# Optimization experiments

Hardware: AMD Instinct MI355X
Metric: run time of the kernel (lower is better)

The kernel has to match this reference:

```python
import jax, jax.numpy as jnp
import numpy as np

N_NODES = 100000
N_EDGES = 1600000
D_IN = 256
D_OUT = 64
BN_EPS = 1e-5


def setup_inputs() -> dict:
    key = jax.random.key(0)
    ks = jax.random.split(key, 8)
    x = jax.random.normal(ks[0], (N_NODES, D_IN), dtype=jnp.float32)
    edge_index = jax.random.randint(ks[1], (2, N_EDGES), 0, N_NODES, dtype=jnp.int32)
    W = jax.random.normal(ks[2], (D_OUT, D_IN), dtype=jnp.float32) / np.sqrt(D_IN).astype(np.float32)
    bias = 0.01 * jax.random.normal(ks[3], (D_OUT,), dtype=jnp.float32)
    gamma = 1.0 + 0.1 * jax.random.normal(ks[4], (D_OUT,), dtype=jnp.float32)
    beta = 0.1 * jax.random.normal(ks[5], (D_OUT,), dtype=jnp.float32)
    running_mean = 0.1 * jax.random.normal(ks[6], (D_OUT,), dtype=jnp.float32)
    running_var = jax.random.uniform(ks[7], (D_OUT,), dtype=jnp.float32, minval=0.5, maxval=1.5)
    return {"x": x, "edge_index": edge_index, "W": W, "bias": bias,
            "gamma": gamma, "beta": beta,
            "running_mean": running_mean, "running_var": running_var}


def reference(x, edge_index, W, bias, gamma, beta, running_mean, running_var):
    # GCNConv (PyG semantics): transform -> symmetric-normalized scatter-add with
    # self-loops (edge_weight = ones, self-loop weight = 1), then +bias.
    n = x.shape[0]
    loop = jnp.arange(n, dtype=edge_index.dtype)
    row = jnp.concatenate([edge_index[0], loop])  # source nodes
    col = jnp.concatenate([edge_index[1], loop])  # target nodes
    w = jnp.ones(row.shape[0], dtype=x.dtype)
    deg = jax.ops.segment_sum(w, col, num_segments=n)          # [N]
    dinv = jnp.where(deg > 0, jax.lax.rsqrt(deg), 0.0)          # D^{-1/2}
    norm = dinv[row] * w * dinv[col]                            # [E+N]
    xw = x @ W.T                                                # [N, D_OUT]
    agg = jax.ops.segment_sum(norm[:, None] * xw[row], col, num_segments=n)
    out = agg + bias
    # BatchNorm1d in eval mode (running stats); dropout inactive in eval.
    out = (out - running_mean) * jax.lax.rsqrt(running_var + BN_EPS) * gamma + beta
    return jax.nn.relu(out)
```

## Files before the change

kernel.cpp:

```cpp
#include <hip/hip_runtime.h>
#include <hip/hip_bf16.h>

#define D_IN 256
#define D_OUT 64
#define BN_EPS 1e-5f

#define BINSHIFT 8
#define BINCAP 4608
#define PCHUNK 8192

typedef __attribute__((ext_vector_type(4))) float floatx4;
typedef __attribute__((ext_vector_type(8))) __bf16 bf16x8;
typedef __attribute__((ext_vector_type(4))) unsigned uintx4;

__global__ __launch_bounds__(256) void k_prep(
        const float* __restrict__ W, __bf16* __restrict__ whi, __bf16* __restrict__ wlo,
        const float* __restrict__ bias, const float* __restrict__ gamma,
        const float* __restrict__ beta, const float* __restrict__ rmean,
        const float* __restrict__ rvar,
        float* __restrict__ bnsc, float* __restrict__ bnsh,
        int* __restrict__ bincur, int nbins) {
    int b = blockIdx.x, t = threadIdx.x;
    if (b < 2) {
        int i = b * 256 + t;
        if (i < nbins) bincur[i] = 0;
        if (b == 1 && t < D_OUT) {
            float sc = rsqrtf(rvar[t] + BN_EPS) * gamma[t];
            bnsc[t] = sc;
            bnsh[t] = (bias[t] - rmean[t]) * sc + beta[t];
        }
        return;
    }
    int tid = (b - 2) * 256 + t;
    int lane = tid & 63, c = (tid >> 6) & 7, tt = tid >> 9;
    int row = tt * 16 + (lane & 15);
    int k0 = c * 32 + (lane >> 4) * 8;
    size_t dst = (size_t)tid * 8;
    #pragma unroll
    for (int j = 0; j < 8; ++j) {
        float w = W[(size_t)row * D_IN + k0 + j];
        __bf16 h = (__bf16)w;
        whi[dst + j] = h;
        wlo[dst + j] = (__bf16)(w - (float)h);
    }
}

__global__ __launch_bounds__(256) void k_part(
        const int* __restrict__ ei, int* __restrict__ bincur,
        unsigned* __restrict__ pairs, int E, int nbins) {
    __shared__ int hist[512];
    __shared__ int base[512];
    int t = threadIdx.x;
    int e0 = blockIdx.x * PCHUNK;

    for (int j = t; j < nbins; j += 256) hist[j] = 0;
    __syncthreads();

    int cols[PCHUNK / 256];
    int ranks[PCHUNK / 256];
    #pragma unroll
    for (int i = 0; i < PCHUNK / 256; ++i) {
        int e = e0 + i * 256 + t;
        if (e < E) {
            int c = ei[E + e];
            cols[i] = c;
            ranks[i] = atomicAdd(&hist[c >> BINSHIFT], 1);
        }
    }
    __syncthreads();
    for (int j = t; j < nbins; j += 256)
        base[j] = atomicAdd(&bincur[j], hist[j]);
    __syncthreads();
    #pragma unroll
    for (int i = 0; i < PCHUNK / 256; ++i) {
        int e = e0 + i * 256 + t;
        if (e < E) {
            int c = cols[i];
            int bin = c >> BINSHIFT;
            int pos = base[bin] + ranks[i];
            if (pos >= BINCAP) pos = BINCAP - 1;
            pairs[(size_t)bin * BINCAP + pos] =
                ((unsigned)ei[e] << 8) | (unsigned)(c & 255);
        }
    }
}

__global__ __launch_bounds__(256) void k_fill3(
        const unsigned* __restrict__ pairs, const int* __restrict__ bincur,
        int* __restrict__ off, float* __restrict__ dinv,
        int* __restrict__ srcs, int n, int nbins) {
    __shared__ int hist[256];
    __shared__ int sc[256];
    __shared__ int curs[256];
    __shared__ int sbase;
    int bin = blockIdx.x, t = threadIdx.x;

    int i0 = 2 * t, i1 = 2 * t + 1;
    int v0 = (i0 < nbins) ? bincur[i0] : 0;
    int v1 = (i1 < nbins) ? bincur[i1] : 0;
    int s = v0 + v1;
    sc[t] = s;
    hist[t] = 0;
    __syncthreads();
    for (int o = 1; o < 256; o <<= 1) {
        int v = (t >= o) ? sc[t - o] : 0;
        __syncthreads();
        sc[t] += v;
        __syncthreads();
    }
    int excl = sc[t] - s;
    if (t == (bin >> 1)) sbase = (bin & 1) ? (excl + v0) : excl;
    if (bin == 0 && t == 255) off[n] = sc[255];
    __syncthreads();
    int binoff_b = sbase;

    int cnt = bincur[bin];
    const unsigned* bp = pairs + (size_t)bin * BINCAP;
    for (int p = t; p < cnt; p += 256)
        atomicAdd(&hist[bp[p] & 255u], 1);
    __syncthreads();
    int own = hist[t];
    sc[t] = own;
    __syncthreads();
    for (int o = 1; o < 256; o <<= 1) {
        int v = (t >= o) ? sc[t - o] : 0;
        __syncthreads();
        sc[t] += v;
        __syncthreads();
    }
    int base = binoff_b + sc[t] - own;
    int node = (bin << BINSHIFT) + t;
    curs[t] = base;
    if (node < n) {
        off[node] = base;
        dinv[node] = rsqrtf((float)(own + 1));
    }
    __syncthreads();
    for (int p = t; p < cnt; p += 256) {
        unsigned v = bp[p];
        int pos = atomicAdd(&curs[v & 255u], 1);
        srcs[pos] = (int)(v >> 8);
    }
}

__global__ __launch_bounds__(256) void k_gemm(
        const float* __restrict__ x, const __bf16* __restrict__ whi,
        const __bf16* __restrict__ wlo, const float* __restrict__ dinv,
        __bf16* __restrict__ yb, int n) {
    int wave = threadIdx.x >> 6;
    int lane = threadIdx.x & 63;
    int m0 = blockIdx.x * 64 + wave * 16;
    if (m0 >= n) return;
    int q = lane >> 4, cl = lane & 15;
    int arow = m0 + cl; if (arow >= n) arow = n - 1;
    const float* ap = x + (size_t)arow * D_IN + q * 8;

    floatx4 acc[4] = {{0.f,0.f,0.f,0.f},{0.f,0.f,0.f,0.f},
                      {0.f,0.f,0.f,0.f},{0.f,0.f,0.f,0.f}};

    #pragma unroll
    for (int c = 0; c < 8; ++c) {
        floatx4 a0 = *(const floatx4*)(ap + c * 32);
        floatx4 a1 = *(const floatx4*)(ap + c * 32 + 4);
        bf16x8 ahi, alo;
        #pragma unroll
        for (int j = 0; j < 4; ++j) {
            __bf16 h0 = (__bf16)a0[j];
            __bf16 h1 = (__bf16)a1[j];
            ahi[j] = h0;     alo[j] = (__bf16)(a0[j] - (float)h0);
            ahi[4 + j] = h1; alo[4 + j] = (__bf16)(a1[j] - (float)h1);
        }
        #pragma unroll
        for (int t = 0; t < 4; ++t) {
            size_t fo = ((size_t)(t * 8 + c) * 64 + lane) * 8;
            bf16x8 bh = *(const bf16x8*)(whi + fo);
            bf16x8 bl = *(const bf16x8*)(wlo + fo);
            acc[t] = __builtin_amdgcn_mfma_f32_16x16x32_bf16(ahi, bh, acc[t], 0, 0, 0);
            acc[t] = __builtin_amdgcn_mfma_f32_16x16x32_bf16(alo, bh, acc[t], 0, 0, 0);
            acc[t] = __builtin_amdgcn_mfma_f32_16x16x32_bf16(ahi, bl, acc[t], 0, 0, 0);
        }
    }

    int nb = m0 + q * 4;
    float dv[4];
    #pragma unroll
    for (int r = 0; r < 4; ++r) dv[r] = (nb + r < n) ? dinv[nb + r] : 0.f;
    #pragma unroll
    for (int t = 0; t < 4; ++t) {
        #pragma unroll
        for (int r = 0; r < 4; ++r) {
            int node = nb + r;
            if (node < n)
                yb[(size_t)node * D_OUT + t * 16 + cl] = (__bf16)(dv[r] * acc[t][r]);
        }
    }
}

__device__ __forceinline__ void acc_row4(uintx4 v, float (&a)[8]) {
    #pragma unroll
    for (int k = 0; k < 4; ++k) {
        a[2 * k]     += __uint_as_float(v[k] << 16);
        a[2 * k + 1] += __uint_as_float(v[k] & 0xffff0000u);
    }
}

__global__ __launch_bounds__(256) void k_aggregate(
        const int* __restrict__ off, const int* __restrict__ srcs,
        const unsigned* __restrict__ ybf, const float* __restrict__ dinv,
        const float* __restrict__ bnsc, const float* __restrict__ bnsh,
        float* __restrict__ out, int n) {
    int node = blockIdx.x * 4 + (threadIdx.x >> 6);
    if (node >= n) return;
    int lane = threadIdx.x & 63;
    int g = lane >> 3, sl = lane & 7;
    int s = off[node], e2 = off[node + 1];

    float a[8] = {0.f, 0.f, 0.f, 0.f, 0.f, 0.f, 0.f, 0.f};
    float dv = 0.f;
    floatx4 bs0, bs1, bh0, bh1;
    if (g == 0) {
        dv = dinv[node];
        bs0 = *(const floatx4*)(bnsc + sl * 8);
        bs1 = *(const floatx4*)(bnsc + sl * 8 + 4);
        bh0 = *(const floatx4*)(bnsh + sl * 8);
        bh1 = *(const floatx4*)(bnsh + sl * 8 + 4);
        uintx4 v = *(const uintx4*)(ybf + (size_t)node * 32 + sl * 4);
        acc_row4(v, a);
    }

    int e = s + g;
    for (; e + 24 < e2; e += 32) {
        int r0 = srcs[e], r1 = srcs[e + 8], r2 = srcs[e + 16], r3 = srcs[e + 24];
        uintx4 v0 = *(const uintx4*)(ybf + (size_t)r0 * 32 + sl * 4);
        uintx4 v1 = *(const uintx4*)(ybf + (size_t)r1 * 32 + sl * 4);
        uintx4 v2 = *(const uintx4*)(ybf + (size_t)r2 * 32 + sl * 4);
        uintx4 v3 = *(const uintx4*)(ybf + (size_t)r3 * 32 + sl * 4);
        acc_row4(v0, a);
        acc_row4(v1, a);
        acc_row4(v2, a);
        acc_row4(v3, a);
    }
    for (; e + 8 < e2; e += 16) {
        int r0 = srcs[e], r1 = srcs[e + 8];
        uintx4 v0 = *(const uintx4*)(ybf + (size_t)r0 * 32 + sl * 4);
        uintx4 v1 = *(const uintx4*)(ybf + (size_t)r1 * 32 + sl * 4);
        acc_row4(v0, a);
        acc_row4(v1, a);
    }
    for (; e < e2; e += 8) {
        uintx4 v = *(const uintx4*)(ybf + (size_t)srcs[e] * 32 + sl * 4);
        acc_row4(v, a);
    }

    #pragma unroll
    for (int k = 0; k < 8; ++k) {
        a[k] += __shfl_xor(a[k], 8);
        a[k] += __shfl_xor(a[k], 16);
        a[k] += __shfl_xor(a[k], 32);
    }

    if (g == 0) {
        float o[8];
        #pragma unroll
        for (int k = 0; k < 4; ++k) {
            o[k]     = fmaf(dv * a[k],     bs0[k], bh0[k]);
            o[4 + k] = fmaf(dv * a[4 + k], bs1[k], bh1[k]);
        }
        floatx4 w0 = { fmaxf(o[0], 0.f), fmaxf(o[1], 0.f),
                       fmaxf(o[2], 0.f), fmaxf(o[3], 0.f) };
        floatx4 w1 = { fmaxf(o[4], 0.f), fmaxf(o[5], 0.f),
                       fmaxf(o[6], 0.f), fmaxf(o[7], 0.f) };
        *(floatx4*)(out + (size_t)node * D_OUT + sl * 8) = w0;
        *(floatx4*)(out + (size_t)node * D_OUT + sl * 8 + 4) = w1;
    }
}

static inline char* align_up(char* p, size_t a) {
    return (char*)(((uintptr_t)p + a - 1) & ~(uintptr_t)(a - 1));
}

extern "C" void kernel_launch(void* const* d_in, const int* in_sizes, int n_in,
                              void* d_out, int out_size, void* d_ws, size_t ws_size,
                              hipStream_t stream) {
    const float* x     = (const float*)d_in[0];
    const int*   ei    = (const int*)d_in[1];
    const float* W     = (const float*)d_in[2];
    const float* bias  = (const float*)d_in[3];
    const float* gamma = (const float*)d_in[4];
    const float* beta  = (const float*)d_in[5];
    const float* rmean = (const float*)d_in[6];
    const float* rvar  = (const float*)d_in[7];
    float* out = (float*)d_out;

    int N = in_sizes[0] / D_IN;
    int E = in_sizes[1] / 2;
    int nbins = (N + (1 << BINSHIFT) - 1) >> BINSHIFT;

    char* p = (char*)d_ws;
    int*      bincur = (int*)p;         p += 512 * 4;
    int*      off    = (int*)p;         p += (size_t)(N + 1) * 4; p = align_up(p, 256);
    float*    dinv   = (float*)p;       p += (size_t)N * 4;       p = align_up(p, 256);
    float*    bnsc   = (float*)p;       p += D_OUT * 4;
    float*    bnsh   = (float*)p;       p += D_OUT * 4;           p = align_up(p, 256);
    __bf16*   whi    = (__bf16*)p;      p += (size_t)D_OUT * D_IN * 2; p = align_up(p, 256);
    __bf16*   wlo    = (__bf16*)p;      p += (size_t)D_OUT * D_IN * 2; p = align_up(p, 256);
    __bf16*   yb     = (__bf16*)p;      p += (size_t)N * D_OUT * 2;    p = align_up(p, 256);
    int*      srcs   = (int*)p;         p += (size_t)E * 4;       p = align_up(p, 256);
    unsigned* pairs  = (unsigned*)p;

    k_prep<<<10, 256, 0, stream>>>(W, whi, wlo, bias, gamma, beta, rmean, rvar,
                                   bnsc, bnsh, bincur, nbins);
    k_part<<<(E + PCHUNK - 1) / PCHUNK, 256, 0, stream>>>(ei, bincur, pairs, E, nbins);
    k_fill3<<<nbins, 256, 0, stream>>>(pairs, bincur, off, dinv, srcs, N, nbins);
    k_gemm<<<(N + 63) / 64, 256, 0, stream>>>(x, whi, wlo, dinv, yb, N);
    k_aggregate<<<(N + 3) / 4, 256, 0, stream>>>(off, srcs, (const unsigned*)yb,
                                                 dinv, bnsc, bnsh, out, N);
}
```

Before: 287.0 us.

## Drop CSR build; aggregate directly from 64-node bins with LDS atomics

```diff
diff --git a/kernel.cpp b/kernel.cpp
--- a/kernel.cpp
+++ b/kernel.cpp
@@ -5,8 +5,8 @@
 #define D_OUT 64
 #define BN_EPS 1e-5f
 
-#define BINSHIFT 8
-#define BINCAP 4608
+#define BINSHIFT 6
+#define BINCAP 1536
 #define PCHUNK 8192
 
 typedef __attribute__((ext_vector_type(4))) float floatx4;
@@ -19,37 +19,45 @@
         const float* __restrict__ beta, const float* __restrict__ rmean,
         const float* __restrict__ rvar,
         float* __restrict__ bnsc, float* __restrict__ bnsh,
-        int* __restrict__ bincur, int nbins) {
+        int* __restrict__ bincur, int* __restrict__ deg, int nbins, int N) {
     int b = blockIdx.x, t = threadIdx.x;
-    if (b < 2) {
+    if (b < 8) {
         int i = b * 256 + t;
         if (i < nbins) bincur[i] = 0;
-        if (b == 1 && t < D_OUT) {
+        return;
+    }
+    if (b == 8) {
+        if (t < D_OUT) {
             float sc = rsqrtf(rvar[t] + BN_EPS) * gamma[t];
             bnsc[t] = sc;
             bnsh[t] = (bias[t] - rmean[t]) * sc + beta[t];
         }
         return;
     }
-    int tid = (b - 2) * 256 + t;
-    int lane = tid & 63, c = (tid >> 6) & 7, tt = tid >> 9;
-    int row = tt * 16 + (lane & 15);
-    int k0 = c * 32 + (lane >> 4) * 8;
-    size_t dst = (size_t)tid * 8;
-    #pragma unroll
-    for (int j = 0; j < 8; ++j) {
-        float w = W[(size_t)row * D_IN + k0 + j];
-        __bf16 h = (__bf16)w;
-        whi[dst + j] = h;
-        wlo[dst + j] = (__bf16)(w - (float)h);
-    }
+    if (b < 17) {
+        int tid = (b - 9) * 256 + t;
+        int lane = tid & 63, c = (tid >> 6) & 7, tt = tid >> 9;
+        int row = tt * 16 + (lane & 15);
+        int k0 = c * 32 + (lane >> 4) * 8;
+        size_t dst = (size_t)tid * 8;
+        #pragma unroll
+        for (int j = 0; j < 8; ++j) {
+            float w = W[(size_t)row * D_IN + k0 + j];
+            __bf16 h = (__bf16)w;
+            whi[dst + j] = h;
+            wlo[dst + j] = (__bf16)(w - (float)h);
+        }
+        return;
+    }
+    int stride = (gridDim.x - 17) * 256;
+    for (int i = (b - 17) * 256 + t; i < N; i += stride) deg[i] = 0;
 }
 
 __global__ __launch_bounds__(256) void k_part(
-        const int* __restrict__ ei, int* __restrict__ bincur,
+        const int* __restrict__ ei, int* __restrict__ bincur, int* __restrict__ deg,
         unsigned* __restrict__ pairs, int E, int nbins) {
-    __shared__ int hist[512];
-    __shared__ int base[512];
+    __shared__ int hist[2048];
+    __shared__ int base[2048];
     int t = threadIdx.x;
     int e0 = blockIdx.x * PCHUNK;
 
@@ -65,11 +73,14 @@
             int c = ei[E + e];
             cols[i] = c;
             ranks[i] = atomicAdd(&hist[c >> BINSHIFT], 1);
-        }
-    }
-    __syncthreads();
-    for (int j = t; j < nbins; j += 256)
-        base[j] = atomicAdd(&bincur[j], hist[j]);
+            atomicAdd(&deg[c], 1);
+        }
+    }
+    __syncthreads();
+    for (int j = t; j < nbins; j += 256) {
+        int h = hist[j];
+        base[j] = h ? atomicAdd(&bincur[j], h) : 0;
+    }
     __syncthreads();
     #pragma unroll
     for (int i = 0; i < PCHUNK / 256; ++i) {
@@ -80,72 +91,14 @@
             int pos = base[bin] + ranks[i];
             if (pos >= BINCAP) pos = BINCAP - 1;
             pairs[(size_t)bin * BINCAP + pos] =
-                ((unsigned)ei[e] << 8) | (unsigned)(c & 255);
-        }
-    }
-}
-
-__global__ __launch_bounds__(256) void k_fill3(
-        const unsigned* __restrict__ pairs, const int* __restrict__ bincur,
-        int* __restrict__ off, float* __restrict__ dinv,
-        int* __restrict__ srcs, int n, int nbins) {
-    __shared__ int hist[256];
-    __shared__ int sc[256];
-    __shared__ int curs[256];
-    __shared__ int sbase;
-    int bin = blockIdx.x, t = threadIdx.x;
-
-    int i0 = 2 * t, i1 = 2 * t + 1;
-    int v0 = (i0 < nbins) ? bincur[i0] : 0;
-    int v1 = (i1 < nbins) ? bincur[i1] : 0;
-    int s = v0 + v1;
-    sc[t] = s;
-    hist[t] = 0;
-    __syncthreads();
-    for (int o = 1; o < 256; o <<= 1) {
-        int v = (t >= o) ? sc[t - o] : 0;
-        __syncthreads();
-        sc[t] += v;
-        __syncthreads();
-    }
-    int excl = sc[t] - s;
-    if (t == (bin >> 1)) sbase = (bin & 1) ? (excl + v0) : excl;
-    if (bin == 0 && t == 255) off[n] = sc[255];
-    __syncthreads();
-    int binoff_b = sbase;
-
-    int cnt = bincur[bin];
-    const unsigned* bp = pairs + (size_t)bin * BINCAP;
-    for (int p = t; p < cnt; p += 256)
-        atomicAdd(&hist[bp[p] & 255u], 1);
-    __syncthreads();
-    int own = hist[t];
-    sc[t] = own;
-    __syncthreads();
-    for (int o = 1; o < 256; o <<= 1) {
-        int v = (t >= o) ? sc[t - o] : 0;
-        __syncthreads();
-        sc[t] += v;
-        __syncthreads();
-    }
-    int base = binoff_b + sc[t] - own;
-    int node = (bin << BINSHIFT) + t;
-    curs[t] = base;
-    if (node < n) {
-        off[node] = base;
-        dinv[node] = rsqrtf((float)(own + 1));
-    }
-    __syncthreads();
-    for (int p = t; p < cnt; p += 256) {
-        unsigned v = bp[p];
-        int pos = atomicAdd(&curs[v & 255u], 1);
-        srcs[pos] = (int)(v >> 8);
+                ((unsigned)ei[e] << BINSHIFT) | (unsigned)(c & 63);
+        }
     }
 }
 
 __global__ __launch_bounds__(256) void k_gemm(
         const float* __restrict__ x, const __bf16* __restrict__ whi,
-        const __bf16* __restrict__ wlo, const float* __restrict__ dinv,
+        const __bf16* __restrict__ wlo, const int* __restrict__ deg,
         __bf16* __restrict__ yb, int n) {
     int wave = threadIdx.x >> 6;
     int lane = threadIdx.x & 63;
@@ -184,7 +137,8 @@
     int nb = m0 + q * 4;
     float dv[4];
     #pragma unroll
-    for (int r = 0; r < 4; ++r) dv[r] = (nb + r < n) ? dinv[nb + r] : 0.f;
+    for (int r = 0; r < 4; ++r)
+        dv[r] = (nb + r < n) ? rsqrtf((float)(deg[nb + r] + 1)) : 0.f;
     #pragma unroll
     for (int t = 0; t < 4; ++t) {
         #pragma unroll
@@ -196,82 +150,74 @@
     }
 }
 
-__device__ __forceinline__ void acc_row4(uintx4 v, float (&a)[8]) {
-    #pragma unroll
-    for (int k = 0; k < 4; ++k) {
-        a[2 * k]     += __uint_as_float(v[k] << 16);
-        a[2 * k + 1] += __uint_as_float(v[k] & 0xffff0000u);
-    }
-}
-
 __global__ __launch_bounds__(256) void k_aggregate(
-        const int* __restrict__ off, const int* __restrict__ srcs,
-        const unsigned* __restrict__ ybf, const float* __restrict__ dinv,
+        const unsigned* __restrict__ pairs, const int* __restrict__ bincur,
+        const int* __restrict__ deg, const unsigned* __restrict__ ybf,
         const float* __restrict__ bnsc, const float* __restrict__ bnsh,
         float* __restrict__ out, int n) {
-    int node = blockIdx.x * 4 + (threadIdx.x >> 6);
-    if (node >= n) return;
-    int lane = threadIdx.x & 63;
-    int g = lane >> 3, sl = lane & 7;
-    int s = off[node], e2 = off[node + 1];
-
-    float a[8] = {0.f, 0.f, 0.f, 0.f, 0.f, 0.f, 0.f, 0.f};
-    float dv = 0.f;
-    floatx4 bs0, bs1, bh0, bh1;
-    if (g == 0) {
-        dv = dinv[node];
-        bs0 = *(const floatx4*)(bnsc + sl * 8);
-        bs1 = *(const floatx4*)(bnsc + sl * 8 + 4);
-        bh0 = *(const floatx4*)(bnsh + sl * 8);
-        bh1 = *(const floatx4*)(bnsh + sl * 8 + 4);
-        uintx4 v = *(const uintx4*)(ybf + (size_t)node * 32 + sl * 4);
-        acc_row4(v, a);
-    }
-
-    int e = s + g;
-    for (; e + 24 < e2; e += 32) {
-        int r0 = srcs[e], r1 = srcs[e + 8], r2 = srcs[e + 16], r3 = srcs[e + 24];
-        uintx4 v0 = *(const uintx4*)(ybf + (size_t)r0 * 32 + sl * 4);
-        uintx4 v1 = *(const uintx4*)(ybf + (size_t)r1 * 32 + sl * 4);
-        uintx4 v2 = *(const uintx4*)(ybf + (size_t)r2 * 32 + sl * 4);
-        uintx4 v3 = *(const uintx4*)(ybf + (size_t)r3 * 32 + sl * 4);
-        acc_row4(v0, a);
-        acc_row4(v1, a);
-        acc_row4(v2, a);
-        acc_row4(v3, a);
-    }
-    for (; e + 8 < e2; e += 16) {
-        int r0 = srcs[e], r1 = srcs[e + 8];
-        uintx4 v0 = *(const uintx4*)(ybf + (size_t)r0 * 32 + sl * 4);
-        uintx4 v1 = *(const uintx4*)(ybf + (size_t)r1 * 32 + sl * 4);
-        acc_row4(v0, a);
-        acc_row4(v1, a);
-    }
-    for (; e < e2; e += 8) {
-        uintx4 v = *(const uintx4*)(ybf + (size_t)srcs[e] * 32 + sl * 4);
-        acc_row4(v, a);
-    }
-
-    #pragma unroll
-    for (int k = 0; k < 8; ++k) {
-        a[k] += __shfl_xor(a[k], 8);
-        a[k] += __shfl_xor(a[k], 16);
-        a[k] += __shfl_xor(a[k], 32);
-    }
-
-    if (g == 0) {
-        float o[8];
+    __shared__ float acc[64][64];
+    int bin = blockIdx.x, t = threadIdx.x;
+
+    float* fa = (float*)acc;
+    #pragma unroll
+    for (int i = 0; i < 16; ++i) fa[t + i * 256] = 0.f;
+    __syncthreads();
+
+    int cnt = bincur[bin]; if (cnt > BINCAP) cnt = BINCAP;
+    const unsigned* bp = pairs + (size_t)bin * BINCAP;
+    int g = t >> 3, sl = t & 7;
+
+    int p = g;
+    for (; p + 32 < cnt; p += 64) {
+        unsigned pr0 = bp[p], pr1 = bp[p + 32];
+        uintx4 v0 = *(const uintx4*)(ybf + (size_t)(pr0 >> BINSHIFT) * 32 + sl * 4);
+        uintx4 v1 = *(const uintx4*)(ybf + (size_t)(pr1 >> BINSHIFT) * 32 + sl * 4);
+        int t0 = pr0 & 63, t1 = pr1 & 63;
         #pragma unroll
         for (int k = 0; k < 4; ++k) {
-            o[k]     = fmaf(dv * a[k],     bs0[k], bh0[k]);
-            o[4 + k] = fmaf(dv * a[4 + k], bs1[k], bh1[k]);
-        }
-        floatx4 w0 = { fmaxf(o[0], 0.f), fmaxf(o[1], 0.f),
-                       fmaxf(o[2], 0.f), fmaxf(o[3], 0.f) };
-        floatx4 w1 = { fmaxf(o[4], 0.f), fmaxf(o[5], 0.f),
-                       fmaxf(o[6], 0.f), fmaxf(o[7], 0.f) };
-        *(floatx4*)(out + (size_t)node * D_OUT + sl * 8) = w0;
-        *(floatx4*)(out + (size_t)node * D_OUT + sl * 8 + 4) = w1;
+            atomicAdd(&acc[t0][sl * 8 + 2 * k],     __uint_as_float(v0[k] << 16));
+            atomicAdd(&acc[t0][sl * 8 + 2 * k + 1], __uint_as_float(v0[k] & 0xffff0000u));
+        }
+        #pragma unroll
+        for (int k = 0; k < 4; ++k) {
+            atomicAdd(&acc[t1][sl * 8 + 2 * k],     __uint_as_float(v1[k] << 16));
+            atomicAdd(&acc[t1][sl * 8 + 2 * k + 1], __uint_as_float(v1[k] & 0xffff0000u));
+        }
+    }
+    for (; p < cnt; p += 32) {
+        unsigned pr = bp[p];
+        uintx4 v = *(const uintx4*)(ybf + (size_t)(pr >> BINSHIFT) * 32 + sl * 4);
+        int tl = pr & 63;
+        #pragma unroll
+        for (int k = 0; k < 4; ++k) {
+            atomicAdd(&acc[tl][sl * 8 + 2 * k],     __uint_as_float(v[k] << 16));
+            atomicAdd(&acc[tl][sl * 8 + 2 * k + 1], __uint_as_float(v[k] & 0xffff0000u));
+        }
+    }
+    __syncthreads();
+
+    int nl = t >> 2, ch0 = (t & 3) * 16;
+    int node = (bin << BINSHIFT) + nl;
+    if (node < n) {
+        float dv = rsqrtf((float)(deg[node] + 1));
+        const unsigned* yr = ybf + (size_t)node * 32 + (t & 3) * 8;
+        #pragma unroll
+        for (int j = 0; j < 4; ++j) {
+            unsigned u0 = yr[2 * j], u1 = yr[2 * j + 1];
+            float s0 = acc[nl][ch0 + 4 * j + 0] + __uint_as_float(u0 << 16);
+            float s1 = acc[nl][ch0 + 4 * j + 1] + __uint_as_float(u0 & 0xffff0000u);
+            float s2 = acc[nl][ch0 + 4 * j + 2] + __uint_as_float(u1 << 16);
+            float s3 = acc[nl][ch0 + 4 * j + 3] + __uint_as_float(u1 & 0xffff0000u);
+            floatx4 bs = *(const floatx4*)(bnsc + ch0 + 4 * j);
+            floatx4 bh = *(const floatx4*)(bnsh + ch0 + 4 * j);
+            float o0 = fmaf(dv * s0, bs[0], bh[0]);
+            float o1 = fmaf(dv * s1, bs[1], bh[1]);
+            float o2 = fmaf(dv * s2, bs[2], bh[2]);
+            float o3 = fmaf(dv * s3, bs[3], bh[3]);
+            floatx4 w = { fmaxf(o0, 0.f), fmaxf(o1, 0.f),
+                          fmaxf(o2, 0.f), fmaxf(o3, 0.f) };
+            *(floatx4*)(out + (size_t)node * D_OUT + ch0 + 4 * j) = w;
+        }
     }
 }
 
@@ -297,22 +243,19 @@
     int nbins = (N + (1 << BINSHIFT) - 1) >> BINSHIFT;
 
     char* p = (char*)d_ws;
-    int*      bincur = (int*)p;         p += 512 * 4;
-    int*      off    = (int*)p;         p += (size_t)(N + 1) * 4; p = align_up(p, 256);
-    float*    dinv   = (float*)p;       p += (size_t)N * 4;       p = align_up(p, 256);
+    int*      bincur = (int*)p;         p += 2048 * 4;
+    int*      deg    = (int*)p;         p += (size_t)N * 4;       p = align_up(p, 256);
     float*    bnsc   = (float*)p;       p += D_OUT * 4;
     float*    bnsh   = (float*)p;       p += D_OUT * 4;           p = align_up(p, 256);
     __bf16*   whi    = (__bf16*)p;      p += (size_t)D_OUT * D_IN * 2; p = align_up(p, 256);
     __bf16*   wlo    = (__bf16*)p;      p += (size_t)D_OUT * D_IN * 2; p = align_up(p, 256);
     __bf16*   yb     = (__bf16*)p;      p += (size_t)N * D_OUT * 2;    p = align_up(p, 256);
-    int*      srcs   = (int*)p;         p += (size_t)E * 4;       p = align_up(p, 256);
     unsigned* pairs  = (unsigned*)p;
 
-    k_prep<<<10, 256, 0, stream>>>(W, whi, wlo, bias, gamma, beta, rmean, rvar,
-                                   bnsc, bnsh, bincur, nbins);
-    k_part<<<(E + PCHUNK - 1) / PCHUNK, 256, 0, stream>>>(ei, bincur, pairs, E, nbins);
-    k_fill3<<<nbins, 256, 0, stream>>>(pairs, bincur, off, dinv, srcs, N, nbins);
-    k_gemm<<<(N + 63) / 64, 256, 0, stream>>>(x, whi, wlo, dinv, yb, N);
-    k_aggregate<<<(N + 3) / 4, 256, 0, stream>>>(off, srcs, (const unsigned*)yb,
-                                                 dinv, bnsc, bnsh, out, N);
-}
+    k_prep<<<115, 256, 0, stream>>>(W, whi, wlo, bias, gamma, beta, rmean, rvar,
+                                    bnsc, bnsh, bincur, deg, nbins, N);
+    k_part<<<(E + PCHUNK - 1) / PCHUNK, 256, 0, stream>>>(ei, bincur, deg, pairs, E, nbins);
+    k_gemm<<<(N + 63) / 64, 256, 0, stream>>>(x, whi, wlo, deg, yb, N);
+    k_aggregate<<<nbins, 256, 0, stream>>>(pairs, bincur, deg, (const unsigned*)yb,
+                                           bnsc, bnsh, out, N);
+}
```

After: 877.0 us. 206% more time.

## Split transformed features into four column slabs and aggregate each in separate passes

Applied to the files above, without the earlier changes.

```diff
diff --git a/kernel.cpp b/kernel.cpp
--- a/kernel.cpp
+++ b/kernel.cpp
@@ -11,7 +11,6 @@
 
 typedef __attribute__((ext_vector_type(4))) float floatx4;
 typedef __attribute__((ext_vector_type(8))) __bf16 bf16x8;
-typedef __attribute__((ext_vector_type(4))) unsigned uintx4;
 
 __global__ __launch_bounds__(256) void k_prep(
         const float* __restrict__ W, __bf16* __restrict__ whi, __bf16* __restrict__ wlo,
@@ -146,7 +145,7 @@
 __global__ __launch_bounds__(256) void k_gemm(
         const float* __restrict__ x, const __bf16* __restrict__ whi,
         const __bf16* __restrict__ wlo, const float* __restrict__ dinv,
-        __bf16* __restrict__ yb, int n) {
+        __bf16* __restrict__ ys, int n) {
     int wave = threadIdx.x >> 6;
     int lane = threadIdx.x & 63;
     int m0 = blockIdx.x * 64 + wave * 16;
@@ -191,87 +190,82 @@
         for (int r = 0; r < 4; ++r) {
             int node = nb + r;
             if (node < n)
-                yb[(size_t)node * D_OUT + t * 16 + cl] = (__bf16)(dv[r] * acc[t][r]);
-        }
-    }
-}
-
-__device__ __forceinline__ void acc_row4(uintx4 v, float (&a)[8]) {
-    #pragma unroll
-    for (int k = 0; k < 4; ++k) {
-        a[2 * k]     += __uint_as_float(v[k] << 16);
-        a[2 * k + 1] += __uint_as_float(v[k] & 0xffff0000u);
-    }
-}
-
-__global__ __launch_bounds__(256) void k_aggregate(
+                ys[((size_t)t * n + node) * 16 + cl] = (__bf16)(dv[r] * acc[t][r]);
+        }
+    }
+}
+
+__device__ __forceinline__ void acc_row(uint2 v, float& a0, float& a1,
+                                        float& a2, float& a3) {
+    a0 += __uint_as_float(v.x << 16);
+    a1 += __uint_as_float(v.x & 0xffff0000u);
+    a2 += __uint_as_float(v.y << 16);
+    a3 += __uint_as_float(v.y & 0xffff0000u);
+}
+
+__global__ __launch_bounds__(256) void k_agg(
         const int* __restrict__ off, const int* __restrict__ srcs,
-        const unsigned* __restrict__ ybf, const float* __restrict__ dinv,
+        const unsigned* __restrict__ yq, const float* __restrict__ dinv,
         const float* __restrict__ bnsc, const float* __restrict__ bnsh,
-        float* __restrict__ out, int n) {
+        float* __restrict__ out, int n, int q) {
     int node = blockIdx.x * 4 + (threadIdx.x >> 6);
     if (node >= n) return;
     int lane = threadIdx.x & 63;
-    int g = lane >> 3, sl = lane & 7;
+    int g = lane >> 2, sl = lane & 3;
     int s = off[node], e2 = off[node + 1];
 
-    float a[8] = {0.f, 0.f, 0.f, 0.f, 0.f, 0.f, 0.f, 0.f};
+    float a0 = 0.f, a1 = 0.f, a2 = 0.f, a3 = 0.f;
     float dv = 0.f;
-    floatx4 bs0, bs1, bh0, bh1;
+    floatx4 bs, bh;
     if (g == 0) {
         dv = dinv[node];
-        bs0 = *(const floatx4*)(bnsc + sl * 8);
-        bs1 = *(const floatx4*)(bnsc + sl * 8 + 4);
-        bh0 = *(const floatx4*)(bnsh + sl * 8);
-        bh1 = *(const floatx4*)(bnsh + sl * 8 + 4);
-        uintx4 v = *(const uintx4*)(ybf + (size_t)node * 32 + sl * 4);
-        acc_row4(v, a);
+        bs = *(const floatx4*)(bnsc + q * 16 + sl * 4);
+        bh = *(const floatx4*)(bnsh + q * 16 + sl * 4);
+        uint2 v = *(const uint2*)(yq + (size_t)node * 8 + sl * 2);
+        acc_row(v, a0, a1, a2, a3);
     }
 
     int e = s + g;
-    for (; e + 24 < e2; e += 32) {
-        int r0 = srcs[e], r1 = srcs[e + 8], r2 = srcs[e + 16], r3 = srcs[e + 24];
-        uintx4 v0 = *(const uintx4*)(ybf + (size_t)r0 * 32 + sl * 4);
-        uintx4 v1 = *(const uintx4*)(ybf + (size_t)r1 * 32 + sl * 4);
-        uintx4 v2 = *(const uintx4*)(ybf + (size_t)r2 * 32 + sl * 4);
-        uintx4 v3 = *(const uintx4*)(ybf + (size_t)r3 * 32 + sl * 4);
-        acc_row4(v0, a);
-        acc_row4(v1, a);
-        acc_row4(v2, a);
-        acc_row4(v3, a);
-    }
-    for (; e + 8 < e2; e += 16) {
-        int r0 = srcs[e], r1 = srcs[e + 8];
-        uintx4 v0 = *(const uintx4*)(ybf + (size_t)r0 * 32 + sl * 4);
-        uintx4 v1 = *(const uintx4*)(ybf + (size_t)r1 * 32 + sl * 4);
-        acc_row4(v0, a);
-        acc_row4(v1, a);
-    }
-    for (; e < e2; e += 8) {
-        uintx4 v = *(const uintx4*)(ybf + (size_t)srcs[e] * 32 + sl * 4);
-        acc_row4(v, a);
-    }
-
-    #pragma unroll
-    for (int k = 0; k < 8; ++k) {
-        a[k] += __shfl_xor(a[k], 8);
-        a[k] += __shfl_xor(a[k], 16);
-        a[k] += __shfl_xor(a[k], 32);
-    }
+    for (; e + 48 < e2; e += 64) {
+        int r0 = srcs[e], r1 = srcs[e + 16], r2 = srcs[e + 32], r3 = srcs[e + 48];
+        uint2 v0 = *(const uint2*)(yq + (size_t)r0 * 8 + sl * 2);
+        uint2 v1 = *(const uint2*)(yq + (size_t)r1 * 8 + sl * 2);
+        uint2 v2 = *(const uint2*)(yq + (size_t)r2 * 8 + sl * 2);
+        uint2 v3 = *(const uint2*)(yq + (size_t)r3 * 8 + sl * 2);
+        acc_row(v0, a0, a1, a2, a3);
+        acc_row(v1, a0, a1, a2, a3);
+        acc_row(v2, a0, a1, a2, a3);
+        acc_row(v3, a0, a1, a2, a3);
+    }
+    for (; e + 16 < e2; e += 32) {
+        int r0 = srcs[e], r1 = srcs[e + 16];
+        uint2 v0 = *(const uint2*)(yq + (size_t)r0 * 8 + sl * 2);
+        uint2 v1 = *(const uint2*)(yq + (size_t)r1 * 8 + sl * 2);
+        acc_row(v0, a0, a1, a2, a3);
+        acc_row(v1, a0, a1, a2, a3);
+    }
+    for (; e < e2; e += 16) {
+        uint2 v = *(const uint2*)(yq + (size_t)srcs[e] * 8 + sl * 2);
+        acc_row(v, a0, a1, a2, a3);
+    }
+
+    a0 += __shfl_xor(a0, 4);  a1 += __shfl_xor(a1, 4);
+    a2 += __shfl_xor(a2, 4);  a3 += __shfl_xor(a3, 4);
+    a0 += __shfl_xor(a0, 8);  a1 += __shfl_xor(a1, 8);
+    a2 += __shfl_xor(a2, 8);  a3 += __shfl_xor(a3, 8);
+    a0 += __shfl_xor(a0, 16); a1 += __shfl_xor(a1, 16);
+    a2 += __shfl_xor(a2, 16); a3 += __shfl_xor(a3, 16);
+    a0 += __shfl_xor(a0, 32); a1 += __shfl_xor(a1, 32);
+    a2 += __shfl_xor(a2, 32); a3 += __shfl_xor(a3, 32);
 
     if (g == 0) {
-        float o[8];
-        #pragma unroll
-        for (int k = 0; k < 4; ++k) {
-            o[k]     = fmaf(dv * a[k],     bs0[k], bh0[k]);
-            o[4 + k] = fmaf(dv * a[4 + k], bs1[k], bh1[k]);
-        }
-        floatx4 w0 = { fmaxf(o[0], 0.f), fmaxf(o[1], 0.f),
-                       fmaxf(o[2], 0.f), fmaxf(o[3], 0.f) };
-        floatx4 w1 = { fmaxf(o[4], 0.f), fmaxf(o[5], 0.f),
-                       fmaxf(o[6], 0.f), fmaxf(o[7], 0.f) };
-        *(floatx4*)(out + (size_t)node * D_OUT + sl * 8) = w0;
-        *(floatx4*)(out + (size_t)node * D_OUT + sl * 8 + 4) = w1;
+        float o0 = fmaf(dv * a0, bs[0], bh[0]);
+        float o1 = fmaf(dv * a1, bs[1], bh[1]);
+        float o2 = fmaf(dv * a2, bs[2], bh[2]);
+        float o3 = fmaf(dv * a3, bs[3], bh[3]);
+        floatx4 o = { o0 > 0.f ? o0 : 0.f, o1 > 0.f ? o1 : 0.f,
+                      o2 > 0.f ? o2 : 0.f, o3 > 0.f ? o3 : 0.f };
+        *(floatx4*)(out + (size_t)node * D_OUT + q * 16 + sl * 4) = o;
     }
 }
 
@@ -304,7 +298,7 @@
     float*    bnsh   = (float*)p;       p += D_OUT * 4;           p = align_up(p, 256);
     __bf16*   whi    = (__bf16*)p;      p += (size_t)D_OUT * D_IN * 2; p = align_up(p, 256);
     __bf16*   wlo    = (__bf16*)p;      p += (size_t)D_OUT * D_IN * 2; p = align_up(p, 256);
-    __bf16*   yb     = (__bf16*)p;      p += (size_t)N * D_OUT * 2;    p = align_up(p, 256);
+    __bf16*   ys     = (__bf16*)p;      p += (size_t)N * D_OUT * 2;    p = align_up(p, 256);
     int*      srcs   = (int*)p;         p += (size_t)E * 4;       p = align_up(p, 256);
     unsigned* pairs  = (unsigned*)p;
 
@@ -312,7 +306,10 @@
                                    bnsc, bnsh, bincur, nbins);
     k_part<<<(E + PCHUNK - 1) / PCHUNK, 256, 0, stream>>>(ei, bincur, pairs, E, nbins);
     k_fill3<<<nbins, 256, 0, stream>>>(pairs, bincur, off, dinv, srcs, N, nbins);
-    k_gemm<<<(N + 63) / 64, 256, 0, stream>>>(x, whi, wlo, dinv, yb, N);
-    k_aggregate<<<(N + 3) / 4, 256, 0, stream>>>(off, srcs, (const unsigned*)yb,
-                                                 dinv, bnsc, bnsh, out, N);
-}
+    k_gemm<<<(N + 63) / 64, 256, 0, stream>>>(x, whi, wlo, dinv, ys, N);
+    for (int q = 0; q < 4; ++q) {
+        const unsigned* yq = (const unsigned*)(ys + (size_t)q * N * 16);
+        k_agg<<<(N + 3) / 4, 256, 0, stream>>>(off, srcs, yq, dinv,
+                                               bnsc, bnsh, out, N, q);
+    }
+}
```

After: 368.7 us. +28.5%, slower.
